# Performance work log

Hardware: AMD Instinct MI355X
Metric: run time of the kernel (lower is better)

The kernel has to match this reference:

```python
import jax, jax.numpy as jnp
import numpy as np

VOCAB = 100000
EMB = 128
B = 16384
C = 20
N = 20


def setup_inputs() -> dict:
    key = jax.random.key(0)
    k1, k2, k3, k4, k5 = jax.random.split(key, 5)
    initrange = 1.0 / EMB
    return {
        "pos_target": jax.random.randint(k1, (B,), 0, VOCAB),
        "pos_contexts": jax.random.randint(k2, (B, C), 0, VOCAB),
        "pos_negatives": jax.random.randint(k3, (B, N), 0, VOCAB),
        "context_table": jax.random.uniform(k4, (VOCAB, EMB), jnp.float32, -initrange, initrange),
        "output_table": jax.random.uniform(k5, (VOCAB, EMB), jnp.float32, -initrange, initrange),
    }


def reference(pos_target, pos_contexts, pos_negatives, context_table, output_table):
    # gather + sum over context window: [B, C, D] -> [B, D]
    mean_contexts = jnp.sum(context_table[pos_contexts], axis=1)
    emb_target = output_table[pos_target]           # [B, D]
    emb_negs = output_table[pos_negatives]          # [B, N, D]

    # positive objective: dot(mean_contexts, emb_target) per row
    pos_score = jnp.clip(jnp.sum(mean_contexts * emb_target, axis=1), -10.0, 10.0)
    objective = -jax.nn.log_sigmoid(pos_score)      # [B]

    # negative objective: bmm [B,N,D] x [B,D] -> [B,N]
    neg_score = jnp.clip(jnp.einsum("bnd,bd->bn", emb_negs, mean_contexts), -10.0, 10.0)
    neg_objective = -jnp.sum(jax.nn.log_sigmoid(-neg_score), axis=1)  # [B]

    return jnp.mean(objective + neg_objective)
```

## Files before the change

### kernel.cpp

```cpp
#include <hip/hip_runtime.h>
#include <math.h>

#define VOCAB 100000
#define EMB   128
#define BATCH 16384
#define CTX   20
#define NEG   20
#define NSCORE (NEG + 1)

__device__ __forceinline__ float dot4(float4 a, float4 b) {
    return fmaf(a.x, b.x, fmaf(a.y, b.y, fmaf(a.z, b.z, a.w * b.w)));
}

__device__ __forceinline__ float fast_softplus(float x) {
    return __logf(1.0f + __expf(x));
}

__global__ __launch_bounds__(256, 4) void cbow_loss_kernel(
    const int*   __restrict__ pos_target,
    const int*   __restrict__ pos_contexts,
    const int*   __restrict__ pos_negatives,
    const float* __restrict__ context_table,
    const float* __restrict__ output_table,
    float*       __restrict__ out)
{
    const int tid  = threadIdx.x;
    const int lane = tid & 63;
    const int wave = tid >> 6;
    const int half = lane >> 5;
    const int sub  = lane & 31;

    const int row = blockIdx.x * 8 + wave * 2 + half;

    const float4* ctab = (const float4*)context_table;
    const float4* otab = (const float4*)output_table;

    int cidx_l = (sub < CTX) ? pos_contexts[row * CTX + sub] : 0;
    int sidx_l = (sub < NSCORE)
                     ? (sub == 0 ? pos_target[row]
                                 : pos_negatives[row * NEG + (sub - 1)])
                     : 0;

    float4 acc = make_float4(0.f, 0.f, 0.f, 0.f);
#pragma unroll
    for (int g = 0; g < 2; ++g) {
        float4 vb[10];
#pragma unroll
        for (int j = 0; j < 10; ++j) {
            const int idx = __shfl(cidx_l, g * 10 + j, 32);
            vb[j] = ctab[idx * 32 + sub];
        }
#pragma unroll
        for (int j = 0; j < 10; ++j) {
            acc.x += vb[j].x; acc.y += vb[j].y;
            acc.z += vb[j].z; acc.w += vb[j].w;
        }
    }

    float part[NSCORE];
#pragma unroll
    for (int g = 0; g < 3; ++g) {
        float4 vb[7];
#pragma unroll
        for (int j = 0; j < 7; ++j) {
            const int idx = __shfl(sidx_l, g * 7 + j, 32);
            vb[j] = otab[idx * 32 + sub];
        }
#pragma unroll
        for (int j = 0; j < 7; ++j) part[g * 7 + j] = dot4(acc, vb[j]);
    }

#pragma unroll
    for (int s = 16; s >= 1; s >>= 1) {
#pragma unroll
        for (int n = 0; n < NSCORE; ++n) part[n] += __shfl_xor(part[n], s);
    }

    float ps = fminf(fmaxf(part[0], -10.f), 10.f);
    float loss = fast_softplus(-ps);
#pragma unroll
    for (int n = 1; n < NSCORE; ++n) {
        float ns = fminf(fmaxf(part[n], -10.f), 10.f);
        loss += fast_softplus(ns);
    }

    __shared__ float sdata[8];
    if (sub == 0) sdata[wave * 2 + half] = loss;
    __syncthreads();
    if (tid == 0) {
        float s = 0.f;
#pragma unroll
        for (int i = 0; i < 8; ++i) s += sdata[i];
        atomicAdd(out, s * (1.0f / (float)BATCH));
    }
}

extern "C" void kernel_launch(void* const* d_in, const int* in_sizes, int n_in,
                              void* d_out, int out_size, void* d_ws, size_t ws_size,
                              hipStream_t stream) {
    const int*   pos_target    = (const int*)d_in[0];
    const int*   pos_contexts  = (const int*)d_in[1];
    const int*   pos_negatives = (const int*)d_in[2];
    const float* context_table = (const float*)d_in[3];
    const float* output_table  = (const float*)d_in[4];
    float* out = (float*)d_out;

    hipMemsetAsync(out, 0, sizeof(float), stream);

    const int rows_per_block = 8;
    const int grid = BATCH / rows_per_block;
    cbow_loss_kernel<<<grid, 256, 0, stream>>>(
        pos_target, pos_contexts, pos_negatives, context_table, output_table, out);
}
```

Baseline: 153.9 us.

## Map each batch row to 16 lanes with double-buffered gathers

Each row is now handled by 16 lanes instead of 32, and each lane loads two float4 chunks per embedding row, so every block covers 16 rows and the grid is halved. The context and score gathers are split into groups, with the next group's loads issued before the current group is accumulated, to keep more memory requests in flight. This raises register pressure from the two double-buffered arrays under launch_bounds(256,4), which could cause spills or reduce occupancy.

```diff
diff --git a/kernel.cpp b/kernel.cpp
--- a/kernel.cpp
+++ b/kernel.cpp
@@ -27,51 +27,85 @@
     const int tid  = threadIdx.x;
     const int lane = tid & 63;
     const int wave = tid >> 6;
-    const int half = lane >> 5;
-    const int sub  = lane & 31;
+    const int q    = lane >> 4;
+    const int sub  = lane & 15;
 
-    const int row = blockIdx.x * 8 + wave * 2 + half;
+    const int row = blockIdx.x * 16 + wave * 4 + q;
 
     const float4* ctab = (const float4*)context_table;
     const float4* otab = (const float4*)output_table;
 
-    int cidx_l = (sub < CTX) ? pos_contexts[row * CTX + sub] : 0;
-    int sidx_l = (sub < NSCORE)
-                     ? (sub == 0 ? pos_target[row]
-                                 : pos_negatives[row * NEG + (sub - 1)])
-                     : 0;
+    int cidx0 = pos_contexts[row * CTX + sub];
+    int cidx1 = (sub < CTX - 16) ? pos_contexts[row * CTX + 16 + sub] : 0;
+    int sidx0 = (sub == 0) ? pos_target[row]
+                           : pos_negatives[row * NEG + sub - 1];
+    int sidx1 = (sub < NSCORE - 16) ? pos_negatives[row * NEG + 15 + sub] : 0;
 
-    float4 acc = make_float4(0.f, 0.f, 0.f, 0.f);
+    auto ctx_idx = [&](int j) {
+        return (j < 16) ? __shfl(cidx0, j, 16) : __shfl(cidx1, j - 16, 16);
+    };
+    auto sc_idx = [&](int j) {
+        return (j < 16) ? __shfl(sidx0, j, 16) : __shfl(sidx1, j - 16, 16);
+    };
+
+    float4 alo = make_float4(0.f, 0.f, 0.f, 0.f);
+    float4 ahi = make_float4(0.f, 0.f, 0.f, 0.f);
+    {
+        float4 lo[2][5], hi[2][5];
 #pragma unroll
-    for (int g = 0; g < 2; ++g) {
-        float4 vb[10];
-#pragma unroll
-        for (int j = 0; j < 10; ++j) {
-            const int idx = __shfl(cidx_l, g * 10 + j, 32);
-            vb[j] = ctab[idx * 32 + sub];
+        for (int j = 0; j < 5; ++j) {
+            const int idx = ctx_idx(j);
+            lo[0][j] = ctab[idx * 32 + sub];
+            hi[0][j] = ctab[idx * 32 + 16 + sub];
         }
 #pragma unroll
-        for (int j = 0; j < 10; ++j) {
-            acc.x += vb[j].x; acc.y += vb[j].y;
-            acc.z += vb[j].z; acc.w += vb[j].w;
+        for (int g = 0; g < 4; ++g) {
+            if (g + 1 < 4) {
+#pragma unroll
+                for (int j = 0; j < 5; ++j) {
+                    const int idx = ctx_idx((g + 1) * 5 + j);
+                    lo[(g + 1) & 1][j] = ctab[idx * 32 + sub];
+                    hi[(g + 1) & 1][j] = ctab[idx * 32 + 16 + sub];
+                }
+            }
+#pragma unroll
+            for (int j = 0; j < 5; ++j) {
+                const float4 a = lo[g & 1][j], b = hi[g & 1][j];
+                alo.x += a.x; alo.y += a.y; alo.z += a.z; alo.w += a.w;
+                ahi.x += b.x; ahi.y += b.y; ahi.z += b.z; ahi.w += b.w;
+            }
         }
     }
 
     float part[NSCORE];
-#pragma unroll
-    for (int g = 0; g < 3; ++g) {
-        float4 vb[7];
+    {
+        float4 slo[2][7], shi[2][7];
 #pragma unroll
         for (int j = 0; j < 7; ++j) {
-            const int idx = __shfl(sidx_l, g * 7 + j, 32);
-            vb[j] = otab[idx * 32 + sub];
+            const int idx = sc_idx(j);
+            slo[0][j] = otab[idx * 32 + sub];
+            shi[0][j] = otab[idx * 32 + 16 + sub];
         }
 #pragma unroll
-        for (int j = 0; j < 7; ++j) part[g * 7 + j] = dot4(acc, vb[j]);
+        for (int g = 0; g < 3; ++g) {
+            if (g + 1 < 3) {
+#pragma unroll
+                for (int j = 0; j < 7; ++j) {
+                    const int idx = sc_idx((g + 1) * 7 + j);
+                    slo[(g + 1) & 1][j] = otab[idx * 32 + sub];
+                    shi[(g + 1) & 1][j] = otab[idx * 32 + 16 + sub];
+                }
+            }
+#pragma unroll
+            for (int j = 0; j < 7; ++j) {
+                part[g * 7 + j] =
+                    dot4(alo, slo[g & 1][j]) + dot4(ahi, shi[g & 1][j]);
+            }
+        }
     }
 
 #pragma unroll
-    for (int s = 16; s >= 1; s >>= 1) {
+    for (int s = 8; s >= 1; s >>= 1) {
 #pragma unroll
         for (int n = 0; n < NSCORE; ++n) part[n] += __shfl_xor(part[n], s);
     }
@@ -84,13 +118,13 @@
         loss += fast_softplus(ns);
     }
 
-    __shared__ float sdata[8];
-    if (sub == 0) sdata[wave * 2 + half] = loss;
+    __shared__ float sdata[16];
+    if (sub == 0) sdata[wave * 4 + q] = loss;
     __syncthreads();
     if (tid == 0) {
         float s = 0.f;
 #pragma unroll
-        for (int i = 0; i < 8; ++i) s += sdata[i];
+        for (int i = 0; i < 16; ++i) s += sdata[i];
         atomicAdd(out, s * (1.0f / (float)BATCH));
     }
 }
@@ -107,7 +141,7 @@
 
     hipMemsetAsync(out, 0, sizeof(float), stream);
 
-    const int rows_per_block = 8;
+    const int rows_per_block = 16;
     const int grid = BATCH / rows_per_block;
     cbow_loss_kernel<<<grid, 256, 0, stream>>>(
         pos_target, pos_contexts, pos_negatives, context_table, output_table, out);
```

After: 151.0 us. Within noise of the previous version (-1.9%).
